# Optimization experiments

Measured on AMD Instinct MI355X. Metric: run time of the kernel, lower is better.

## Reference

```python
import jax, jax.numpy as jnp
import numpy as np

B, S, D, H, L = 2048, 23, 768, 8, 50
HD = D // H  # head dim = 96
NEG = -1e9


def setup_inputs() -> dict:
    key = jax.random.key(0)
    ks = jax.random.split(key, 9)
    sc = 0.02
    return {
        "cls_embeddings": jax.random.normal(ks[0], (B, S, D), jnp.float32),
        "exist_mask": jax.random.randint(ks[1], (B, S), 0, 2, jnp.int32),
        "missing_table": jax.random.normal(ks[2], (S, D), jnp.float32) * sc,
        "in_proj_w": jax.random.normal(ks[3], (3 * D, D), jnp.float32) * sc,
        "in_proj_b": jax.random.normal(ks[4], (3 * D,), jnp.float32) * sc,
        "out_proj_w": jax.random.normal(ks[5], (D, D), jnp.float32) * sc,
        "out_proj_b": jax.random.normal(ks[6], (D,), jnp.float32) * sc,
        "pred_w": jax.random.normal(ks[7], (L, D), jnp.float32) * sc,
        "pred_b": jax.random.normal(ks[8], (L,), jnp.float32) * sc,
    }


def reference(cls_embeddings, exist_mask, missing_table, in_proj_w, in_proj_b,
              out_proj_w, out_proj_b, pred_w, pred_b):
    exist = exist_mask.astype(bool)  # [B,S] True where section present
    # Build section_embeddings: BERT CLS where present, learned missing emb otherwise
    base = jnp.where(exist[..., None], cls_embeddings, missing_table[None])  # [B,S,D]

    # nn.MultiheadAttention: shared in_proj then split into q,k,v
    qkv = base @ in_proj_w.T + in_proj_b          # [B,S,3D]
    q, k, v = jnp.split(qkv, 3, axis=-1)
    q = q.reshape(B, S, H, HD) * (1.0 / np.sqrt(HD))
    k = k.reshape(B, S, H, HD)
    v = v.reshape(B, S, H, HD)

    # single-query attention per missing section over EXISTING sections only
    scores = jnp.einsum('bqhd,bkhd->bhqk', q, k)  # [B,H,S,S]
    scores = jnp.where(exist[:, None, None, :], scores, NEG)
    attn = jax.nn.softmax(scores, axis=-1)
    ctx = jnp.einsum('bhqk,bkhd->bqhd', attn, v).reshape(B, S, D)
    attn_out = ctx @ out_proj_w.T + out_proj_b    # [B,S,D]

    # existing sections keep their CLS embedding; if an EHR has NO existing
    # sections the original code skips it entirely (keeps missing embeddings)
    any_exist = exist.any(axis=1)[:, None, None]  # [B,1,1]
    keep = exist[..., None] | ~any_exist
    section_embeddings = jnp.where(keep, base, attn_out)

    document_embeddings = section_embeddings.mean(axis=1)  # [B,D]
    logits = document_embeddings @ pred_w.T + pred_b       # [B,L]
    return logits
```

## Files before the change

kernel.cpp:

```cpp
#include <hip/hip_runtime.h>
#include <hip/hip_bf16.h>


typedef unsigned short u16;
typedef unsigned int u32;
typedef __attribute__((ext_vector_type(8))) short sh8;
typedef __attribute__((ext_vector_type(4))) float f32x4;

#define BB 2048
#define SS 23
#define DD 768
#define HH 8
#define HDIM 96
#define LL 50
#define NN 1024
#define NCAP 26624
#define MTILES 208

__device__ __forceinline__ u16 f2bf(float f) {
  u32 u = __float_as_uint(f);
  u32 r = (u + 0x7fffu + ((u >> 16) & 1u)) >> 16;
  return (u16)r;
}
__device__ __forceinline__ float bf2f(u16 h) {
  return __uint_as_float(((u32)h) << 16);
}

__device__ __forceinline__ void gld16(const void* g, void* l) {
  __builtin_amdgcn_global_load_lds((const __attribute__((address_space(1))) void*)g,
                                   (__attribute__((address_space(3))) void*)l, 16, 0, 0);
}

__global__ __launch_bounds__(256) void prep1_kernel(const int* __restrict__ exist,
                                                    const float* __restrict__ inw,
                                                    const float* __restrict__ inb,
                                                    const float* __restrict__ mt,
                                                    int* __restrict__ ex_off,
                                                    u16* __restrict__ Bcomb,
                                                    float* __restrict__ biasc,
                                                    float* __restrict__ qmf) {
  const int idx = blockIdx.x;
  const int t = threadIdx.x;
  if (idx == 0) {
    __shared__ int wtot[4];
    int c[8];
    int tot = 0;
    for (int j = 0; j < 8; ++j) {
      const int b = t * 8 + j;
      int cc = 0;
      for (int s = 0; s < SS; ++s) cc += (exist[b * SS + s] != 0);
      tot += cc;
      c[j] = tot;
    }
    const int lane = t & 63, w = t >> 6;
    int v = tot;
    for (int off = 1; off < 64; off <<= 1) {
      int n = __shfl_up(v, off, 64);
      if (lane >= off) v += n;
    }
    if (lane == 63) wtot[w] = v;
    __syncthreads();
    int wbase = 0;
    for (int i = 0; i < w; ++i) wbase += wtot[i];
    const int excl = wbase + v - tot;
    for (int j = 0; j < 8; ++j) ex_off[t * 8 + j + 1] = excl + c[j];
    if (t == 0) ex_off[0] = 0;
  } else if (idx < 289) {
    const int i = ((idx - 1) * 256 + t) * 8;
    if (i < DD * DD) {
      const float* src = inw + (size_t)2 * DD * DD;
      float4 a = *(const float4*)(src + i);
      float4 b = *(const float4*)(src + i + 4);
      uint4 o;
      o.x = (u32)f2bf(a.x) | ((u32)f2bf(a.y) << 16);
      o.y = (u32)f2bf(a.z) | ((u32)f2bf(a.w) << 16);
      o.z = (u32)f2bf(b.x) | ((u32)f2bf(b.y) << 16);
      o.w = (u32)f2bf(b.z) | ((u32)f2bf(b.w) << 16);
      *(uint4*)((u16*)Bcomb + i) = o;
    }
  } else if (idx < 358) {
    const int q69 = idx - 289;
    const int s = q69 / 3;
    const int o = (q69 % 3) * 256 + t;
    const float* mrow = mt + s * DD;
    const float* wrow = inw + (size_t)o * DD;
    float acc = 0.f;
    for (int d = 0; d < DD; d += 4) {
      float4 a = *(const float4*)(mrow + d);
      float4 b = *(const float4*)(wrow + d);
      acc += a.x * b.x + a.y * b.y + a.z * b.z + a.w * b.w;
    }
    qmf[s * DD + o] = (acc + inb[o]) * 0.10206207261596575f;
  } else {
    for (int i = t; i < NN; i += 256) biasc[i] = (i < DD) ? inb[1536 + i] : 0.f;
  }
}

__global__ __launch_bounds__(256) void prep2_kernel(const float* __restrict__ qmf,
                                                    const float* __restrict__ inw,
                                                    const float* __restrict__ inb,
                                                    const float* __restrict__ pw,
                                                    const float* __restrict__ pb,
                                                    const float* __restrict__ outw,
                                                    const float* __restrict__ outb,
                                                    const float* __restrict__ mt,
                                                    const float* __restrict__ cls,
                                                    const int* __restrict__ exist,
                                                    const int* __restrict__ ex_off,
                                                    u16* __restrict__ Bcomb,
                                                    float* __restrict__ biasc,
                                                    float* __restrict__ Wfold,
                                                    float* __restrict__ boutdot,
                                                    float* __restrict__ logits0,
                                                    u16* __restrict__ Xex,
                                                    float* __restrict__ doc_acc) {
  const int idx = blockIdx.x;
  const int t = threadIdx.x;
  __shared__ float red[2][256];
  __shared__ int exl[SS];
  __shared__ int nE_s;
  if (idx < 552) {
    const int r = idx / 3, chunk = idx - r * 3;
    const int s = r >> 3, h = r & 7;
    const int Dc = chunk * 256 + t;
    const float* q = qmf + s * DD + h * HDIM;
    const float* wk = inw + (size_t)(DD + h * HDIM) * DD + Dc;
    float acc = 0.f;
    for (int d = 0; d < HDIM; ++d)
      acc += q[d] * wk[(size_t)d * DD];
    Bcomb[(size_t)(DD + r) * DD + Dc] = f2bf(acc);
    if (chunk == 0 && t == 0) {
      float bb = 0.f;
      const float* bk = inb + DD + h * HDIM;
      for (int d = 0; d < HDIM; ++d) bb += q[d] * bk[d];
      biasc[DD + r] = bb;
    }
  } else if (idx < 702) {
    const int idx2 = idx - 552;
    const int l = idx2 / 3, chunk = idx2 - l * 3;
    const int din = chunk * 256 + t;
    float acc = 0.f;
    for (int dout = 0; dout < DD; ++dout)
      acc += pw[(size_t)l * DD + dout] * outw[(size_t)dout * DD + din];
    Wfold[(size_t)l * DD + din] = acc;
    if (chunk == 0) {
      float pbd = 0.f, plz = 0.f;
      for (int d = t; d < DD; d += 256) {
        const float pv = pw[(size_t)l * DD + d];
        pbd += pv * outb[d];
        float ms = 0.f;
        for (int s = 0; s < SS; ++s) ms += mt[s * DD + d];
        plz += pv * ms;
      }
      red[0][t] = pbd; red[1][t] = plz;
      __syncthreads();
      for (int s = 128; s > 0; s >>= 1) {
        if (t < s) { red[0][t] += red[0][t + s]; red[1][t] += red[1][t + s]; }
        __syncthreads();
      }
      if (t == 0) { boutdot[l] = red[0][0]; logits0[l] = red[1][0] * (1.f / 23.f) + pb[l]; }
    }
  } else {
    const int b = idx - 702;
    if (t == 0) {
      int n = 0;
      for (int s = 0; s < SS; ++s) if (exist[b * SS + s]) exl[n++] = s;
      nE_s = n;
    }
    __syncthreads();
    const int nE = nE_s;
    const int e0 = ex_off[b];
    if (t < 192) {
      const int d0 = t * 4;
      float a0 = 0.f, a1 = 0.f, a2 = 0.f, a3 = 0.f;
      for (int i = 0; i < nE; ++i) {
        const float* row = cls + (size_t)(b * SS + exl[i]) * DD + d0;
        float4 v = *(const float4*)row;
        a0 += v.x; a1 += v.y; a2 += v.z; a3 += v.w;
        if (e0 + i < NCAP) {
          ushort4 pk;
          pk.x = f2bf(v.x); pk.y = f2bf(v.y); pk.z = f2bf(v.z); pk.w = f2bf(v.w);
          *(ushort4*)(Xex + (size_t)(e0 + i) * DD + d0) = pk;
        }
      }
      float4 outv = {a0, a1, a2, a3};
      *(float4*)(doc_acc + (size_t)b * DD + d0) = outv;
    }
  }
}

__global__ __launch_bounds__(256, 2)
void gemm_bt_kernel(const u16* __restrict__ A, const u16* __restrict__ Bw,
                    const float* __restrict__ bias, u16* __restrict__ Cc,
                    const int* __restrict__ rows_ptr, int N) {
  constexpr int K = 768;
  __shared__ u16 lA[128 * 64];
  __shared__ u16 lB[128 * 64];
  const int m0 = blockIdx.y * 128;
  if (m0 >= rows_ptr[0]) return;
  const int n0 = blockIdx.x * 128;
  const int t = threadIdx.x;
  const int w = t >> 6, l = t & 63;
  const int wr = (w >> 1) * 64, wc = (w & 1) * 64;
  const int r16 = l & 15, kg = l >> 4;

  f32x4 acc[4][4] = {};

  const int srow = t >> 3;
  const int scol = (t & 7) * 8;
  const u16* gA = A + (size_t)(m0 + srow) * K + scol;
  const u16* gB = Bw + (size_t)(n0 + srow) * K + scol;
  u16* lAp = lA + t * 8;
  u16* lBp = lB + t * 8;

  for (int kt = 0; kt < K; kt += 64) {
#pragma unroll
    for (int i = 0; i < 4; ++i) {
      gld16(gA + (size_t)i * 32 * K + kt, lAp + i * 2048);
      gld16(gB + (size_t)i * 32 * K + kt, lBp + i * 2048);
    }
    __syncthreads();
#pragma unroll
    for (int kk = 0; kk < 2; ++kk) {
      sh8 af[4], bfr[4];
      const int kc = kk * 32 + kg * 8;
#pragma unroll
      for (int m = 0; m < 4; ++m) af[m] = *(const sh8*)(lA + (wr + m * 16 + r16) * 64 + kc);
#pragma unroll
      for (int n = 0; n < 4; ++n) bfr[n] = *(const sh8*)(lB + (wc + n * 16 + r16) * 64 + kc);
#pragma unroll
      for (int m = 0; m < 4; ++m)
#pragma unroll
        for (int n = 0; n < 4; ++n)
          acc[m][n] = __builtin_amdgcn_mfma_f32_16x16x32_bf16(af[m], bfr[n], acc[m][n], 0, 0, 0);
    }
    __syncthreads();
  }

#pragma unroll
  for (int m = 0; m < 4; ++m) {
    const int row0 = m0 + wr + m * 16 + kg * 4;
#pragma unroll
    for (int n = 0; n < 4; ++n) {
      const int col = n0 + wc + n * 16 + r16;
      const float bv = bias[col];
#pragma unroll
      for (int j = 0; j < 4; ++j)
        Cc[(size_t)(row0 + j) * N + col] = f2bf(acc[m][n][j] + bv);
    }
  }
}

__global__ __launch_bounds__(256) void attn_final_kernel(const u16* __restrict__ VS,
                                                         const int* __restrict__ exist,
                                                         const int* __restrict__ ex_off,
                                                         const float* __restrict__ doc_acc,
                                                         const float* __restrict__ pw,
                                                         const float* __restrict__ pb,
                                                         const float* __restrict__ Wfold,
                                                         const float* __restrict__ boutdot,
                                                         const float* __restrict__ logits0,
                                                         float* __restrict__ out) {
  const int b = blockIdx.x, t = threadIdx.x;
  __shared__ float sc[SS * HH][25];
  __shared__ float psum[HH][25];
  __shared__ float ctxL[DD];
  __shared__ int mil[SS], cnts[2];
  if (t == 0) {
    int ne = 0, nm = 0;
    for (int s = 0; s < SS; ++s) {
      if (exist[b * SS + s]) ne++; else mil[nm++] = s;
    }
    cnts[0] = ne; cnts[1] = nm;
  }
  __syncthreads();
  const int nE = cnts[0], nM = cnts[1];
  if (nE == 0) {
    if (t < LL) out[(size_t)b * LL + t] = logits0[t];
    return;
  }
  const size_t e0 = (size_t)ex_off[b];

  if (nM > 0) {
    const int ee = t & 31, ig = t >> 5;
    for (int i0 = 0; i0 < nM; i0 += 8) {
      const int i = i0 + ig;
      if (ee < nE && i < nM) {
        sh8 v = *(const sh8*)(VS + (e0 + ee) * NN + DD + mil[i] * 8);
#pragma unroll
        for (int h = 0; h < HH; ++h) sc[i * HH + h][ee] = bf2f((u16)v[h]);
      }
    }
    __syncthreads();

    if (t < nM * HH) {
      float* row = sc[t];
      float mx = row[0];
      for (int e = 1; e < nE; ++e) mx = fmaxf(mx, row[e]);
      float sum = 0.f;
      for (int e = 0; e < nE; ++e) { float p = __expf(row[e] - mx); row[e] = p; sum += p; }
      float inv = 1.f / sum;
      for (int e = 0; e < nE; ++e) row[e] *= inv;
    }
    __syncthreads();

    {
      const int h = t >> 5, e2 = t & 31;
      if (e2 < nE) {
        float a = 0.f;
        for (int i = 0; i < nM; ++i) a += sc[i * HH + h][e2];
        psum[h][e2] = a;
      }
    }
    __syncthreads();

    for (int d = t; d < DD; d += 256) {
      const int h = d / HDIM;
      float acc = 0.f;
      for (int e = 0; e < nE; ++e)
        acc += psum[h][e] * bf2f(VS[(e0 + e) * NN + d]);
      ctxL[d] = acc;
    }
    __syncthreads();
  }

  const int w = t >> 6, lane = t & 63;
  const int d0 = lane * 12;
  const float* db = doc_acc + (size_t)b * DD + d0;
  float docv[12];
  *(float4*)(docv)     = *(const float4*)(db);
  *(float4*)(docv + 4) = *(const float4*)(db + 4);
  *(float4*)(docv + 8) = *(const float4*)(db + 8);
  float ctxv[12];
  if (nM > 0) {
#pragma unroll
    for (int j = 0; j < 12; ++j) ctxv[j] = ctxL[d0 + j];
  }
  for (int l = w; l < LL; l += 4) {
    const float* pwl = pw + (size_t)l * DD + d0;
    float acc = 0.f;
    if (nM > 0) {
      const float* wfl = Wfold + (size_t)l * DD + d0;
#pragma unroll
      for (int j = 0; j < 12; ++j) acc += docv[j] * pwl[j] + ctxv[j] * wfl[j];
    } else {
#pragma unroll
      for (int j = 0; j < 12; ++j) acc += docv[j] * pwl[j];
    }
#pragma unroll
    for (int m = 1; m < 64; m <<= 1) acc += __shfl_xor(acc, m, 64);
    if (lane == 0)
      out[(size_t)b * LL + l] = (acc + (float)nM * boutdot[l]) * (1.f / 23.f) + pb[l];
  }
}

extern "C" void kernel_launch(void* const* d_in, const int* in_sizes, int n_in,
                              void* d_out, int out_size, void* d_ws, size_t ws_size,
                              hipStream_t stream) {
  const float* cls  = (const float*)d_in[0];
  const int*   exm  = (const int*)d_in[1];
  const float* mt   = (const float*)d_in[2];
  const float* inw  = (const float*)d_in[3];
  const float* inb  = (const float*)d_in[4];
  const float* outw = (const float*)d_in[5];
  const float* outb = (const float*)d_in[6];
  const float* pw   = (const float*)d_in[7];
  const float* pb   = (const float*)d_in[8];
  float* out = (float*)d_out;

  char* ws = (char*)d_ws;
  size_t off = 0;
  auto alloc = [&](size_t bytes) {
    size_t cur = (off + 255) & ~(size_t)255;
    off = cur + bytes;
    return ws + cur;
  };
  int*   ex_off  = (int*)alloc((BB + 1) * sizeof(int));
  float* qmf     = (float*)alloc((size_t)SS * DD * 4);
  u16*   Bcomb   = (u16*)alloc((size_t)NN * DD * 2);
  float* biasc   = (float*)alloc((size_t)NN * 4);
  float* Wfold   = (float*)alloc((size_t)LL * DD * 4);
  float* boutdot = (float*)alloc((size_t)LL * 4);
  float* logits0 = (float*)alloc((size_t)LL * 4);
  float* doc_acc = (float*)alloc((size_t)BB * DD * 4);
  u16*   Xex     = (u16*)alloc((size_t)NCAP * DD * 2);
  u16*   VS      = (u16*)alloc((size_t)NCAP * NN * 2);

  prep1_kernel<<<359, 256, 0, stream>>>(exm, inw, inb, mt, ex_off, Bcomb, biasc, qmf);
  prep2_kernel<<<2750, 256, 0, stream>>>(qmf, inw, inb, pw, pb, outw, outb, mt, cls,
                                         exm, ex_off, Bcomb, biasc, Wfold, boutdot,
                                         logits0, Xex, doc_acc);
  gemm_bt_kernel<<<dim3(NN / 128, MTILES), 256, 0, stream>>>(Xex, Bcomb, biasc, VS,
                                                             ex_off + BB, NN);
  attn_final_kernel<<<BB, 256, 0, stream>>>(VS, exm, ex_off, doc_acc, pw, pb, Wfold,
                                            boutdot, logits0, out);
}
```

Measured before the change: 390.8 us.

## Split prep2 work into finer blocks using a precomputed row map and atomic Wfold

Computes a global row map of existing sections in prep1, so prep2 can gather and convert each existing CLS row to bf16 in its own block instead of one block per batch walking the rows serially. The document-sum reduction becomes separate per-column blocks. The Wfold fold (pred_w times out_proj_w) is split over four K-chunks and accumulated with atomicAdd into a buffer zeroed in prep1, and the bias-dot/logit reductions get their own blocks. The aim is to remove the long serial tails in prep2 by raising parallelism, at the cost of many more tiny blocks, reading the CLS rows twice, and non-deterministic float atomics.

```diff
diff --git a/kernel.cpp b/kernel.cpp
--- a/kernel.cpp
+++ b/kernel.cpp
@@ -17,6 +17,12 @@
 #define NCAP 26624
 #define MTILES 208
 
+#define G_GATHER 26624
+#define G_DOC    (G_GATHER + 6144)
+#define G_GROW   (G_DOC + 552)
+#define G_WFOLD  (G_GROW + 600)
+#define G_LOG    (G_WFOLD + 50)
+
 __device__ __forceinline__ u16 f2bf(float f) {
   u32 u = __float_as_uint(f);
   u32 r = (u + 0x7fffu + ((u >> 16) & 1u)) >> 16;
@@ -36,21 +42,19 @@
                                                     const float* __restrict__ inb,
                                                     const float* __restrict__ mt,
                                                     int* __restrict__ ex_off,
+                                                    int* __restrict__ rowmap,
                                                     u16* __restrict__ Bcomb,
                                                     float* __restrict__ biasc,
-                                                    float* __restrict__ qmf) {
+                                                    float* __restrict__ qmf,
+                                                    float* __restrict__ Wfold) {
   const int idx = blockIdx.x;
   const int t = threadIdx.x;
   if (idx == 0) {
     __shared__ int wtot[4];
-    int c[8];
     int tot = 0;
     for (int j = 0; j < 8; ++j) {
       const int b = t * 8 + j;
-      int cc = 0;
-      for (int s = 0; s < SS; ++s) cc += (exist[b * SS + s] != 0);
-      tot += cc;
-      c[j] = tot;
+      for (int s = 0; s < SS; ++s) tot += (exist[b * SS + s] != 0);
     }
     const int lane = t & 63, w = t >> 6;
     int v = tot;
@@ -62,22 +66,28 @@
     __syncthreads();
     int wbase = 0;
     for (int i = 0; i < w; ++i) wbase += wtot[i];
-    const int excl = wbase + v - tot;
-    for (int j = 0; j < 8; ++j) ex_off[t * 8 + j + 1] = excl + c[j];
+    int base = wbase + v - tot;
+    for (int j = 0; j < 8; ++j) {
+      const int b = t * 8 + j;
+      for (int s = 0; s < SS; ++s)
+        if (exist[b * SS + s]) {
+          if (base < NCAP) rowmap[base] = b * SS + s;
+          ++base;
+        }
+      ex_off[b + 1] = base;
+    }
     if (t == 0) ex_off[0] = 0;
   } else if (idx < 289) {
     const int i = ((idx - 1) * 256 + t) * 8;
-    if (i < DD * DD) {
-      const float* src = inw + (size_t)2 * DD * DD;
-      float4 a = *(const float4*)(src + i);
-      float4 b = *(const float4*)(src + i + 4);
-      uint4 o;
-      o.x = (u32)f2bf(a.x) | ((u32)f2bf(a.y) << 16);
-      o.y = (u32)f2bf(a.z) | ((u32)f2bf(a.w) << 16);
-      o.z = (u32)f2bf(b.x) | ((u32)f2bf(b.y) << 16);
-      o.w = (u32)f2bf(b.z) | ((u32)f2bf(b.w) << 16);
-      *(uint4*)((u16*)Bcomb + i) = o;
-    }
+    const float* src = inw + (size_t)2 * DD * DD;
+    float4 a = *(const float4*)(src + i);
+    float4 b = *(const float4*)(src + i + 4);
+    uint4 o;
+    o.x = (u32)f2bf(a.x) | ((u32)f2bf(a.y) << 16);
+    o.y = (u32)f2bf(a.z) | ((u32)f2bf(a.w) << 16);
+    o.z = (u32)f2bf(b.x) | ((u32)f2bf(b.y) << 16);
+    o.w = (u32)f2bf(b.z) | ((u32)f2bf(b.w) << 16);
+    *(uint4*)((u16*)Bcomb + i) = o;
   } else if (idx < 358) {
     const int q69 = idx - 289;
     const int s = q69 / 3;
@@ -91,8 +101,14 @@
       acc += a.x * b.x + a.y * b.y + a.z * b.z + a.w * b.w;
     }
     qmf[s * DD + o] = (acc + inb[o]) * 0.10206207261596575f;
+  } else if (idx == 358) {
+    for (int i = t; i < NN; i += 256) biasc[i] = (i < DD) ? inb[1536 + i] : 0.f;
   } else {
-    for (int i = t; i < NN; i += 256) biasc[i] = (i < DD) ? inb[1536 + i] : 0.f;
+    const int i4 = (idx - 359) * 256 + t;
+    if (i4 < (LL * DD) / 4) {
+      float4 z = {0.f, 0.f, 0.f, 0.f};
+      *(float4*)(Wfold + i4 * 4) = z;
+    }
   }
 }
 
@@ -107,6 +123,7 @@
                                                     const float* __restrict__ cls,
                                                     const int* __restrict__ exist,
                                                     const int* __restrict__ ex_off,
+                                                    const int* __restrict__ rowmap,
                                                     u16* __restrict__ Bcomb,
                                                     float* __restrict__ biasc,
                                                     float* __restrict__ Wfold,
@@ -116,11 +133,29 @@
                                                     float* __restrict__ doc_acc) {
   const int idx = blockIdx.x;
   const int t = threadIdx.x;
-  __shared__ float red[2][256];
-  __shared__ int exl[SS];
-  __shared__ int nE_s;
-  if (idx < 552) {
-    const int r = idx / 3, chunk = idx - r * 3;
+  if (idx < G_GATHER) {
+    const int r = idx;
+    if (r >= ex_off[BB]) return;
+    const int m = rowmap[r];
+    if (t < 192) {
+      const int d0 = t * 4;
+      float4 v = *(const float4*)(cls + (size_t)m * DD + d0);
+      ushort4 pk;
+      pk.x = f2bf(v.x); pk.y = f2bf(v.y); pk.z = f2bf(v.z); pk.w = f2bf(v.w);
+      *(ushort4*)(Xex + (size_t)r * DD + d0) = pk;
+    }
+  } else if (idx < G_DOC) {
+    const int id = idx - G_GATHER;
+    const int b = id / 3;
+    const int d = (id % 3) * 256 + t;
+    const float* cb = cls + (size_t)b * SS * DD + d;
+    float acc = 0.f;
+    for (int s = 0; s < SS; ++s)
+      if (exist[b * SS + s]) acc += cb[(size_t)s * DD];
+    doc_acc[(size_t)b * DD + d] = acc;
+  } else if (idx < G_GROW) {
+    const int id = idx - G_DOC;
+    const int r = id / 3, chunk = id - r * 3;
     const int s = r >> 3, h = r & 7;
     const int Dc = chunk * 256 + t;
     const float* q = qmf + s * DD + h * HDIM;
@@ -135,57 +170,36 @@
       for (int d = 0; d < HDIM; ++d) bb += q[d] * bk[d];
       biasc[DD + r] = bb;
     }
-  } else if (idx < 702) {
-    const int idx2 = idx - 552;
-    const int l = idx2 / 3, chunk = idx2 - l * 3;
-    const int din = chunk * 256 + t;
+  } else if (idx < G_WFOLD) {
+    const int id = idx - G_GROW;
+    const int l = id / 12, rem = id % 12;
+    const int din = (rem % 3) * 256 + t;
+    const int dc0 = (rem / 3) * 192;
+    const float* pwl = pw + (size_t)l * DD;
+    const float* ow = outw + (size_t)dc0 * DD + din;
     float acc = 0.f;
-    for (int dout = 0; dout < DD; ++dout)
-      acc += pw[(size_t)l * DD + dout] * outw[(size_t)dout * DD + din];
-    Wfold[(size_t)l * DD + din] = acc;
-    if (chunk == 0) {
-      float pbd = 0.f, plz = 0.f;
-      for (int d = t; d < DD; d += 256) {
-        const float pv = pw[(size_t)l * DD + d];
-        pbd += pv * outb[d];
-        float ms = 0.f;
-        for (int s = 0; s < SS; ++s) ms += mt[s * DD + d];
-        plz += pv * ms;
-      }
-      red[0][t] = pbd; red[1][t] = plz;
+#pragma unroll 8
+    for (int j = 0; j < 192; ++j)
+      acc += pwl[dc0 + j] * ow[(size_t)j * DD];
+    atomicAdd(&Wfold[(size_t)l * DD + din], acc);
+  } else {
+    __shared__ float red[2][256];
+    const int l = idx - G_WFOLD;
+    float pbd = 0.f, plz = 0.f;
+    for (int d = t; d < DD; d += 256) {
+      const float pv = pw[(size_t)l * DD + d];
+      pbd += pv * outb[d];
+      float ms = 0.f;
+      for (int s = 0; s < SS; ++s) ms += mt[s * DD + d];
+      plz += pv * ms;
+    }
+    red[0][t] = pbd; red[1][t] = plz;
+    __syncthreads();
+    for (int s = 128; s > 0; s >>= 1) {
+      if (t < s) { red[0][t] += red[0][t + s]; red[1][t] += red[1][t + s]; }
       __syncthreads();
-      for (int s = 128; s > 0; s >>= 1) {
-        if (t < s) { red[0][t] += red[0][t + s]; red[1][t] += red[1][t + s]; }
-        __syncthreads();
-      }
-      if (t == 0) { boutdot[l] = red[0][0]; logits0[l] = red[1][0] * (1.f / 23.f) + pb[l]; }
-    }
-  } else {
-    const int b = idx - 702;
-    if (t == 0) {
-      int n = 0;
-      for (int s = 0; s < SS; ++s) if (exist[b * SS + s]) exl[n++] = s;
-      nE_s = n;
-    }
-    __syncthreads();
-    const int nE = nE_s;
-    const int e0 = ex_off[b];
-    if (t < 192) {
-      const int d0 = t * 4;
-      float a0 = 0.f, a1 = 0.f, a2 = 0.f, a3 = 0.f;
-      for (int i = 0; i < nE; ++i) {
-        const float* row = cls + (size_t)(b * SS + exl[i]) * DD + d0;
-        float4 v = *(const float4*)row;
-        a0 += v.x; a1 += v.y; a2 += v.z; a3 += v.w;
-        if (e0 + i < NCAP) {
-          ushort4 pk;
-          pk.x = f2bf(v.x); pk.y = f2bf(v.y); pk.z = f2bf(v.z); pk.w = f2bf(v.w);
-          *(ushort4*)(Xex + (size_t)(e0 + i) * DD + d0) = pk;
-        }
-      }
-      float4 outv = {a0, a1, a2, a3};
-      *(float4*)(doc_acc + (size_t)b * DD + d0) = outv;
-    }
+    }
+    if (t == 0) { boutdot[l] = red[0][0]; logits0[l] = red[1][0] * (1.f / 23.f) + pb[l]; }
   }
 }
 
@@ -376,6 +390,7 @@
     return ws + cur;
   };
   int*   ex_off  = (int*)alloc((BB + 1) * sizeof(int));
+  int*   rowmap  = (int*)alloc((size_t)NCAP * sizeof(int));
   float* qmf     = (float*)alloc((size_t)SS * DD * 4);
   u16*   Bcomb   = (u16*)alloc((size_t)NN * DD * 2);
   float* biasc   = (float*)alloc((size_t)NN * 4);
@@ -386,10 +401,11 @@
   u16*   Xex     = (u16*)alloc((size_t)NCAP * DD * 2);
   u16*   VS      = (u16*)alloc((size_t)NCAP * NN * 2);
 
-  prep1_kernel<<<359, 256, 0, stream>>>(exm, inw, inb, mt, ex_off, Bcomb, biasc, qmf);
-  prep2_kernel<<<2750, 256, 0, stream>>>(qmf, inw, inb, pw, pb, outw, outb, mt, cls,
-                                         exm, ex_off, Bcomb, biasc, Wfold, boutdot,
-                                         logits0, Xex, doc_acc);
+  prep1_kernel<<<397, 256, 0, stream>>>(exm, inw, inb, mt, ex_off, rowmap, Bcomb,
+                                        biasc, qmf, Wfold);
+  prep2_kernel<<<G_LOG, 256, 0, stream>>>(qmf, inw, inb, pw, pb, outw, outb, mt, cls,
+                                          exm, ex_off, rowmap, Bcomb, biasc, Wfold,
+                                          boutdot, logits0, Xex, doc_acc);
   gemm_bt_kernel<<<dim3(NN / 128, MTILES), 256, 0, stream>>>(Xex, Bcomb, biasc, VS,
                                                              ex_off + BB, NN);
   attn_final_kernel<<<BB, 256, 0, stream>>>(VS, exm, ex_off, doc_acc, pw, pb, Wfold,
```

Measured after the change: 389.9 us. Within noise of the previous version (-0.2%).
